# Optimization experiments

Hardware: AMD Instinct MI355X
Metric: run time of the kernel (lower is better)

## Reference

```python
import jax, jax.numpy as jnp
import numpy as np

B, S, E, H, FFN, NQ = 4, 2048, 1024, 16, 4096, 8
DK = E // H
EPS = 1e-5


def setup_inputs() -> dict:
    key = jax.random.key(0)
    ks = jax.random.split(key, 8)
    x = jax.random.normal(ks[0], (B, S, E), dtype=jnp.float32)
    theta = jax.random.normal(ks[1], (NQ,), dtype=jnp.float32)  # RY angles
    w1 = jax.random.normal(ks[2], (FFN, NQ), dtype=jnp.float32) / np.sqrt(NQ)
    b1 = jnp.zeros((FFN,), dtype=jnp.float32)
    w2 = jax.random.normal(ks[3], (E, FFN), dtype=jnp.float32) / np.sqrt(FFN)
    b2 = jnp.zeros((E,), dtype=jnp.float32)
    gamma1 = jnp.ones((E,), dtype=jnp.float32)
    beta1 = jnp.zeros((E,), dtype=jnp.float32)
    gamma2 = jnp.ones((E,), dtype=jnp.float32)
    beta2 = jnp.zeros((E,), dtype=jnp.float32)
    return {"x": x, "theta": theta, "w1": w1, "b1": b1, "w2": w2, "b2": b2,
            "gamma1": gamma1, "beta1": beta1, "gamma2": gamma2, "beta2": beta2}


def _layernorm(h, g, b):
    mu = jnp.mean(h, axis=-1, keepdims=True)
    var = jnp.mean(jnp.square(h - mu), axis=-1, keepdims=True)
    return (h - mu) * jax.lax.rsqrt(var + EPS) * g + b


def _attention(x):
    # q = k = v = separate_heads(x); no projection weights in the original.
    q = x.reshape(B, S, H, DK).transpose(0, 2, 1, 3)  # [B,H,S,DK]
    scores = jnp.einsum("bhqd,bhkd->bhqk", q, q) / np.sqrt(DK)
    probs = jax.nn.softmax(scores, axis=-1)
    out = jnp.einsum("bhqk,bhkd->bhqd", probs, q)
    return out.transpose(0, 2, 1, 3).reshape(B, S, E)


def _ffn_quantum(h, theta, w1, b1, w2, b2):
    # Per-token circuit: RX(x_i) then RY(theta_i) on independent qubits,
    # measure PauliZ -> <Z_i> = cos(x_i) * cos(theta_i). Batched over all tokens.
    qout = jnp.cos(h[..., :NQ]) * jnp.cos(theta)  # [B,S,NQ]
    hid = jax.nn.relu(jnp.einsum("bsq,fq->bsf", qout, w1) + b1)
    return jnp.einsum("bsf,ef->bse", hid, w2) + b2


def reference(x, theta, w1, b1, w2, b2, gamma1, beta1, gamma2, beta2):
    attn_out = _attention(x)
    h = _layernorm(x + attn_out, gamma1, beta1)
    ffn_out = _ffn_quantum(h, theta, w1, b1, w2, b2)
    return _layernorm(h + ffn_out, gamma2, beta2)
```

## Files before the change

kernel.cpp:

```cpp
#include <hip/hip_runtime.h>


#define Bq 4
#define Sq 2048
#define Eq 1024
#define Hq 16
#define DKq 64
#define FFNq 4096
#define NQq 8
#define LOG2E 1.44269504f

typedef unsigned int u32;
typedef unsigned short u16;
typedef _Float16 f16;
typedef f16 f16x8 __attribute__((ext_vector_type(8)));
typedef __fp16 fp16x2 __attribute__((ext_vector_type(2)));
typedef float f32x4 __attribute__((ext_vector_type(4)));

#if __has_builtin(__builtin_amdgcn_exp2f)
#define EXP2F __builtin_amdgcn_exp2f
#else
#define EXP2F exp2f
#endif

#define MFMA(a, b, c) __builtin_amdgcn_mfma_f32_16x16x32_f16((a), (b), (c), 0, 0, 0)

#define GLL(g, l)                                                          \
  __builtin_amdgcn_global_load_lds(                                        \
      (const __attribute__((address_space(1))) u32*)(g),                   \
      (__attribute__((address_space(3))) u32*)(l), 16, 0, 0)

__device__ __forceinline__ u16 f2h(float x) {
  f16 t = (f16)x;
  return __builtin_bit_cast(u16, t);
}
__device__ __forceinline__ float h2f(u16 w) {
  return (float)__builtin_bit_cast(f16, w);
}
#if __has_builtin(__builtin_amdgcn_cvt_pkrtz)
__device__ __forceinline__ u32 pkrtz(float a, float b) {
  fp16x2 r = __builtin_amdgcn_cvt_pkrtz(a, b);
  return __builtin_bit_cast(u32, r);
}
#else
__device__ __forceinline__ u32 pkrtz(float a, float b) {
  return (u32)f2h(a) | ((u32)f2h(b) << 16);
}
#endif

union F8 { f16x8 v; u32 w[4]; u16 h[8]; f16 e[8]; };

__global__ void k_cvt(const float* __restrict__ src, uint4* __restrict__ dst, int n8) {
  int i = blockIdx.x * 256 + threadIdx.x;
  if (i >= n8) return;
  const float4* s = (const float4*)src + 2 * (long)i;
  float4 a = s[0], b = s[1];
  uint4 r;
  r.x = pkrtz(a.x, a.y);
  r.y = pkrtz(a.z, a.w);
  r.z = pkrtz(b.x, b.y);
  r.w = pkrtz(b.z, b.w);
  dst[i] = r;
}

__global__ void k_prep(const float* __restrict__ x, u16* __restrict__ xh,
                       u16* __restrict__ xt) {
  __shared__ u16 tile[64 * 72];
  const int tid = threadIdx.x;
  const int bx = blockIdx.x;
  const int sb = bx & 31, bh = bx >> 5;
  const int b = bh >> 4, h = bh & 15;
  const int s0 = sb * 64;
  const int r = tid >> 2, cq = tid & 3;
  const float* xp = x + ((long)(b * Sq + s0 + r)) * Eq + h * 64 + cq * 16;
  float4 f0 = ((const float4*)xp)[0], f1 = ((const float4*)xp)[1];
  float4 f2 = ((const float4*)xp)[2], f3 = ((const float4*)xp)[3];
  u32 w[8];
  w[0] = pkrtz(f0.x, f0.y); w[1] = pkrtz(f0.z, f0.w);
  w[2] = pkrtz(f1.x, f1.y); w[3] = pkrtz(f1.z, f1.w);
  w[4] = pkrtz(f2.x, f2.y); w[5] = pkrtz(f2.z, f2.w);
  w[6] = pkrtz(f3.x, f3.y); w[7] = pkrtz(f3.z, f3.w);
  uint4* xo = (uint4*)(xh + ((long)(b * Sq + s0 + r)) * Eq + h * 64 + cq * 16);
  xo[0] = make_uint4(w[0], w[1], w[2], w[3]);
  xo[1] = make_uint4(w[4], w[5], w[6], w[7]);
  uint4* tp = (uint4*)(tile + r * 72 + cq * 16);
  tp[0] = make_uint4(w[0], w[1], w[2], w[3]);
  tp[1] = make_uint4(w[4], w[5], w[6], w[7]);
  __syncthreads();
  const int d = tid >> 2, rq = tid & 3;
  u32 o[8];
#pragma unroll
  for (int i = 0; i < 8; ++i) {
    u32 lo = tile[(rq * 16 + 2 * i) * 72 + d];
    u32 hi = tile[(rq * 16 + 2 * i + 1) * 72 + d];
    o[i] = lo | (hi << 16);
  }
  uint4* to = (uint4*)(xt + ((long)(bh * 64 + d)) * Sq + s0 + rq * 16);
  to[0] = make_uint4(o[0], o[1], o[2], o[3]);
  to[1] = make_uint4(o[4], o[5], o[6], o[7]);
}

__global__ __launch_bounds__(256, 2) void k_attn(const u16* __restrict__ xh,
                                                 const u16* __restrict__ xt,
                                                 u16* __restrict__ attn) {
  __shared__ __align__(16) u16 lds[32768];
  u16* Pl = lds + 16384;

  const int tid = threadIdx.x;
  const int wave = tid >> 6, lane = tid & 63;
  const int n = lane & 15, quad = lane >> 4;

  const int bx = blockIdx.x;
  const int qb = bx >> 6, bh = bx & 63;
  const int b = bh >> 4, h = bh & 15;

  const u16* xh_bh = xh + (long)b * Sq * Eq + h * 64;
  const u16* xt_bh = xt + (long)bh * 64 * Sq;

  const float SC = 0.125f * LOG2E;
  F8 qf[4][2];
  float shift[4], lrow[4] = {0.f, 0.f, 0.f, 0.f};
#pragma unroll
  for (int nt = 0; nt < 4; ++nt) {
    const int q = qb * 256 + wave * 64 + nt * 16 + n;
    const u16* qp = xh_bh + (long)q * Eq + quad * 8;
    F8 a, c;
    a.v = *(const f16x8*)qp;
    c.v = *(const f16x8*)(qp + 32);
    float s2 = 0.f;
#pragma unroll
    for (int i = 0; i < 8; ++i) {
      float va = (float)a.e[i], vc = (float)c.e[i];
      s2 += va * va + vc * vc;
      qf[nt][0].e[i] = a.e[i] * (f16)SC;
      qf[nt][1].e[i] = c.e[i] * (f16)SC;
    }
    s2 += __shfl_xor(s2, 16);
    s2 += __shfl_xor(s2, 32);
    shift[nt] = SC * s2;
  }

  const int r8 = lane >> 3;
  const int cl = (lane & 7) ^ r8;
  const u16* gK0 = xh_bh + (long)(wave * 16 + r8) * Eq + cl * 8;
  const u16* gK1 = gK0 + 8 * Eq;
  const u16* gV0 = xt_bh + (long)(wave * 16 + r8) * Sq + cl * 8;
  const u16* gV1 = gV0 + 8 * Sq;
  const int lK0 = wave * 1024, lK1 = lK0 + 512;
  const int lV0 = 4096 + wave * 1024, lV1 = lV0 + 512;

  u16* cur = lds;
  u16* nxt = lds + 8192;

  GLL(gK0, cur + lK0); GLL(gK1, cur + lK1);
  GLL(gV0, cur + lV0); GLL(gV1, cur + lV1);
  gK0 += 64 * Eq; gK1 += 64 * Eq; gV0 += 64; gV1 += 64;

  f32x4 O[4][4] = {};
  u16* Pw = Pl + wave * 4096;

  for (int kb = 0; kb < Sq / 64; ++kb) {
    __syncthreads();
    if (kb < Sq / 64 - 1) {
      GLL(gK0, nxt + lK0); GLL(gK1, nxt + lK1);
      GLL(gV0, nxt + lV0); GLL(gV1, nxt + lV1);
      gK0 += 64 * Eq; gK1 += 64 * Eq; gV0 += 64; gV1 += 64;
    }
    u16* Kl = cur;
    u16* Vt = cur + 4096;

    f32x4 ST[4][4];
#pragma unroll
    for (int nt = 0; nt < 4; ++nt) {
      const float ms = -shift[nt];
#pragma unroll
      for (int mt = 0; mt < 4; ++mt) {
        ST[nt][mt][0] = ms; ST[nt][mt][1] = ms;
        ST[nt][mt][2] = ms; ST[nt][mt][3] = ms;
      }
    }
#pragma unroll
    for (int mt = 0; mt < 4; ++mt) {
#pragma unroll
      for (int c = 0; c < 2; ++c) {
        f16x8 af = *(const f16x8*)(Kl + (mt * 16 + n) * 64 +
                                   (((c * 4 + quad) ^ (n & 7)) * 8));
#pragma unroll
        for (int nt = 0; nt < 4; ++nt)
          ST[nt][mt] = MFMA(af, qf[nt][c].v, ST[nt][mt]);
      }
    }

#pragma unroll
    for (int nt = 0; nt < 4; ++nt) {
      float ls = 0.f;
#pragma unroll
      for (int mt = 0; mt < 4; ++mt) {
        float p0 = EXP2F(ST[nt][mt][0]);
        float p1 = EXP2F(ST[nt][mt][1]);
        float p2 = EXP2F(ST[nt][mt][2]);
        float p3 = EXP2F(ST[nt][mt][3]);
        ls += (p0 + p1) + (p2 + p3);
        const int ch = 2 * mt + (quad >> 1);
        *(uint2*)(Pw + nt * 1024 + n * 64 + ((ch ^ (n & 7)) * 8) + (quad & 1) * 4) =
            make_uint2(pkrtz(p0, p1), pkrtz(p2, p3));
      }
      lrow[nt] += ls;
    }

#pragma unroll
    for (int c = 0; c < 2; ++c) {
      const int pc = ((c * 4 + quad) ^ (n & 7)) * 8;
      f16x8 pf[4];
#pragma unroll
      for (int nt = 0; nt < 4; ++nt)
        pf[nt] = *(const f16x8*)(Pw + nt * 1024 + n * 64 + pc);
#pragma unroll
      for (int dt = 0; dt < 4; ++dt) {
        f16x8 vf = *(const f16x8*)(Vt + (dt * 16 + n) * 64 + pc);
#pragma unroll
        for (int nt = 0; nt < 4; ++nt) O[nt][dt] = MFMA(vf, pf[nt], O[nt][dt]);
      }
    }
    u16* t = cur; cur = nxt; nxt = t;
  }

#pragma unroll
  for (int nt = 0; nt < 4; ++nt) {
    float l = lrow[nt];
    l += __shfl_xor(l, 16);
    l += __shfl_xor(l, 32);
    const float inv = 1.0f / l;
    const int q = qb * 256 + wave * 64 + nt * 16 + n;
    u16* op = attn + (long)b * Sq * Eq + (long)q * Eq + h * 64;
#pragma unroll
    for (int dt = 0; dt < 4; ++dt) {
      u32 w0 = pkrtz(O[nt][dt][0] * inv, O[nt][dt][1] * inv);
      u32 w1 = pkrtz(O[nt][dt][2] * inv, O[nt][dt][3] * inv);
      *(uint2*)(op + dt * 16 + quad * 4) = make_uint2(w0, w1);
    }
  }
}

__global__ void k_ln1(const u16* __restrict__ xh, const u16* __restrict__ attn,
                      const float* __restrict__ g, const float* __restrict__ be,
                      const float* __restrict__ theta, u16* __restrict__ hout,
                      u16* __restrict__ qout) {
  const long t = blockIdx.x;
  const int tid = threadIdx.x;
  uint2 xw = ((const uint2*)(xh + t * Eq))[tid];
  uint2 aw = ((const uint2*)(attn + t * Eq))[tid];
  float v0 = h2f(xw.x & 0xffff) + h2f(aw.x & 0xffff);
  float v1 = h2f(xw.x >> 16) + h2f(aw.x >> 16);
  float v2 = h2f(xw.y & 0xffff) + h2f(aw.y & 0xffff);
  float v3 = h2f(xw.y >> 16) + h2f(aw.y >> 16);
  float s = (v0 + v1) + (v2 + v3);
  float s2 = v0 * v0 + v1 * v1 + v2 * v2 + v3 * v3;
#pragma unroll
  for (int o = 1; o < 64; o <<= 1) {
    s += __shfl_xor(s, o);
    s2 += __shfl_xor(s2, o);
  }
  __shared__ float red[8];
  const int wv = tid >> 6, ln = tid & 63;
  if (ln == 0) { red[wv] = s; red[4 + wv] = s2; }
  __syncthreads();
  s = red[0] + red[1] + red[2] + red[3];
  s2 = red[4] + red[5] + red[6] + red[7];
  const float mu = s * (1.f / Eq);
  const float var = s2 * (1.f / Eq) - mu * mu;
  const float rstd = rsqrtf(var + 1e-5f);
  float4 gv = ((const float4*)g)[tid];
  float4 bv = ((const float4*)be)[tid];
  float o0 = (v0 - mu) * rstd * gv.x + bv.x;
  float o1 = (v1 - mu) * rstd * gv.y + bv.y;
  float o2 = (v2 - mu) * rstd * gv.z + bv.z;
  float o3 = (v3 - mu) * rstd * gv.w + bv.w;
  ((uint2*)(hout + t * Eq))[tid] = make_uint2(pkrtz(o0, o1), pkrtz(o2, o3));
  if (tid < 2) {
    float hv[4] = {o0, o1, o2, o3};
    float q[4];
#pragma unroll
    for (int i = 0; i < 4; ++i) q[i] = cosf(hv[i]) * cosf(theta[tid * 4 + i]);
    *(uint2*)(qout + t * NQq + tid * 4) = make_uint2(pkrtz(q[0], q[1]), pkrtz(q[2], q[3]));
  }
}

__global__ void k_hid(const u16* __restrict__ qout, const float* __restrict__ w1,
                      const float* __restrict__ b1, u16* __restrict__ hid) {
  __shared__ float qs[256][8];
  const int tid = threadIdx.x;
  const int fb = blockIdx.x & 63, tb = blockIdx.x >> 6;
  const int f0 = fb * 64, t0 = tb * 256;
  {
    uint4 qw = *(const uint4*)(qout + (long)(t0 + tid) * NQq);
    qs[tid][0] = h2f(qw.x & 0xffff); qs[tid][1] = h2f(qw.x >> 16);
    qs[tid][2] = h2f(qw.y & 0xffff); qs[tid][3] = h2f(qw.y >> 16);
    qs[tid][4] = h2f(qw.z & 0xffff); qs[tid][5] = h2f(qw.z >> 16);
    qs[tid][6] = h2f(qw.w & 0xffff); qs[tid][7] = h2f(qw.w >> 16);
  }
  __syncthreads();
  const int wave = tid >> 6, lane = tid & 63;
  const int f = f0 + lane;
  const float4* wp = (const float4*)(w1 + (long)f * NQq);
  float4 wa = wp[0], wb = wp[1];
  const float bb = b1[f];
  const int trow = wave * 64;
  u16* op = hid + (long)(t0 + trow) * FFNq + f;
#pragma unroll 4
  for (int i = 0; i < 64; ++i) {
    const float* q = qs[trow + i];
    float acc = bb + q[0] * wa.x + q[1] * wa.y + q[2] * wa.z + q[3] * wa.w +
                q[4] * wb.x + q[5] * wb.y + q[6] * wb.z + q[7] * wb.w;
    acc = fmaxf(acc, 0.f);
    op[(long)i * FFNq] = f2h(acc);
  }
}

__global__ __launch_bounds__(256, 2) void k_gemm(const u16* __restrict__ Ah,
                                                 const u16* __restrict__ Bh,
                                                 u16* __restrict__ C) {
  __shared__ __align__(16) u16 lds[32768];
  const int tid = threadIdx.x;
  const int wave = tid >> 6, lane = tid & 63;
  const int n = lane & 15, quad = lane >> 4;
  const int wm = wave >> 1, wn = wave & 1;
  const int m0 = (blockIdx.x >> 3) * 128;
  const int n0 = (blockIdx.x & 7) * 128;
  const int r8 = lane >> 3;
  const int cl = (lane & 7) ^ r8;

  const u16* gA[4];
  const u16* gB[4];
  int lA[4], lB[4];
#pragma unroll
  for (int j = 0; j < 4; ++j) {
    const int row = wave * 32 + j * 8;
    gA[j] = Ah + (long)(m0 + row + r8) * FFNq + cl * 8;
    gB[j] = Bh + (long)(n0 + row + r8) * FFNq + cl * 8;
    lA[j] = row * 64;
    lB[j] = 8192 + row * 64;
  }

  u16* cur = lds;
  u16* nxt = lds + 16384;

#pragma unroll
  for (int j = 0; j < 4; ++j) {
    GLL(gA[j], cur + lA[j]);
    GLL(gB[j], cur + lB[j]);
    gA[j] += 64;
    gB[j] += 64;
  }

  f32x4 acc[4][4] = {};
  for (int it = 0; it < FFNq / 64; ++it) {
    __syncthreads();
    if (it < FFNq / 64 - 1) {
#pragma unroll
      for (int j = 0; j < 4; ++j) {
        GLL(gA[j], nxt + lA[j]);
        GLL(gB[j], nxt + lB[j]);
        gA[j] += 64;
        gB[j] += 64;
      }
    }
    u16* La = cur;
    u16* Lb = cur + 8192;
#pragma unroll
    for (int c = 0; c < 2; ++c) {
      f16x8 af[4], bf[4];
#pragma unroll
      for (int i = 0; i < 4; ++i) {
        const int ra = wm * 64 + i * 16 + n;
        const int rb = wn * 64 + i * 16 + n;
        af[i] = *(const f16x8*)(La + ra * 64 + (((c * 4 + quad) ^ (n & 7)) * 8));
        bf[i] = *(const f16x8*)(Lb + rb * 64 + (((c * 4 + quad) ^ (n & 7)) * 8));
      }
#pragma unroll
      for (int i = 0; i < 4; ++i)
#pragma unroll
        for (int j = 0; j < 4; ++j) acc[i][j] = MFMA(af[i], bf[j], acc[i][j]);
    }
    u16* t = cur; cur = nxt; nxt = t;
  }
#pragma unroll
  for (int i = 0; i < 4; ++i) {
    const int row = m0 + wm * 64 + i * 16 + quad * 4;
#pragma unroll
    for (int j = 0; j < 4; ++j) {
      u16* cp = C + (long)row * Eq + n0 + wn * 64 + j * 16 + n;
      cp[0] = f2h(acc[i][j][0]);
      cp[Eq] = f2h(acc[i][j][1]);
      cp[2 * Eq] = f2h(acc[i][j][2]);
      cp[3 * Eq] = f2h(acc[i][j][3]);
    }
  }
}

__global__ void k_ln2(const u16* __restrict__ hin, const u16* __restrict__ ffn,
                      const float* __restrict__ b2, const float* __restrict__ g,
                      const float* __restrict__ be, float* __restrict__ out) {
  const long t = blockIdx.x;
  const int tid = threadIdx.x;
  uint2 hw = ((const uint2*)(hin + t * Eq))[tid];
  uint2 fw = ((const uint2*)(ffn + t * Eq))[tid];
  float4 b2v = ((const float4*)b2)[tid];
  float v0 = h2f(hw.x & 0xffff) + h2f(fw.x & 0xffff) + b2v.x;
  float v1 = h2f(hw.x >> 16) + h2f(fw.x >> 16) + b2v.y;
  float v2 = h2f(hw.y & 0xffff) + h2f(fw.y & 0xffff) + b2v.z;
  float v3 = h2f(hw.y >> 16) + h2f(fw.y >> 16) + b2v.w;
  float s = (v0 + v1) + (v2 + v3);
  float s2 = v0 * v0 + v1 * v1 + v2 * v2 + v3 * v3;
#pragma unroll
  for (int o = 1; o < 64; o <<= 1) {
    s += __shfl_xor(s, o);
    s2 += __shfl_xor(s2, o);
  }
  __shared__ float red[8];
  const int wv = tid >> 6, ln = tid & 63;
  if (ln == 0) { red[wv] = s; red[4 + wv] = s2; }
  __syncthreads();
  s = red[0] + red[1] + red[2] + red[3];
  s2 = red[4] + red[5] + red[6] + red[7];
  const float mu = s * (1.f / Eq);
  const float var = s2 * (1.f / Eq) - mu * mu;
  const float rstd = rsqrtf(var + 1e-5f);
  float4 gv = ((const float4*)g)[tid];
  float4 bv = ((const float4*)be)[tid];
  float4 o;
  o.x = (v0 - mu) * rstd * gv.x + bv.x;
  o.y = (v1 - mu) * rstd * gv.y + bv.y;
  o.z = (v2 - mu) * rstd * gv.z + bv.z;
  o.w = (v3 - mu) * rstd * gv.w + bv.w;
  ((float4*)(out + t * Eq))[tid] = o;
}

extern "C" void kernel_launch(void* const* d_in, const int* in_sizes, int n_in,
                              void* d_out, int out_size, void* d_ws, size_t ws_size,
                              hipStream_t stream) {
  const float* x = (const float*)d_in[0];
  const float* theta = (const float*)d_in[1];
  const float* w1 = (const float*)d_in[2];
  const float* b1 = (const float*)d_in[3];
  const float* w2 = (const float*)d_in[4];
  const float* b2 = (const float*)d_in[5];
  const float* g1 = (const float*)d_in[6];
  const float* be1 = (const float*)d_in[7];
  const float* g2 = (const float*)d_in[8];
  const float* be2 = (const float*)d_in[9];
  float* out = (float*)d_out;

  char* ws = (char*)d_ws;
  u16* attn = (u16*)(ws);
  u16* h = (u16*)(ws + 16777216);
  u16* xh = (u16*)(ws + 33554432);
  u16* xt = (u16*)(ws + 50331648);
  u16* ffn = (u16*)(ws + 67108864);
  u16* hid = (u16*)(ws + 83886080);
  u16* w2h = (u16*)(ws + 150994944);
  u16* qout = (u16*)(ws + 159383552);

  k_prep<<<Bq * Hq * (Sq / 64), 256, 0, stream>>>(x, xh, xt);
  k_cvt<<<2048, 256, 0, stream>>>(w2, (uint4*)w2h, (Eq * FFNq) / 8);
  k_attn<<<Bq * Hq * (Sq / 256), 256, 0, stream>>>(xh, xt, attn);
  k_ln1<<<Bq * Sq, 256, 0, stream>>>(xh, attn, g1, be1, theta, h, qout);
  k_hid<<<(Bq * Sq / 256) * (FFNq / 64), 256, 0, stream>>>(qout, w1, b1, hid);
  k_gemm<<<(Bq * Sq / 128) * (Eq / 128), 256, 0, stream>>>(hid, w2h, ffn);
  k_ln2<<<Bq * Sq, 256, 0, stream>>>(h, ffn, b2, g2, be2, out);
}
```

Measured before the change: 318.2 us.

## Split attention query tile across 8 waves and add MFMA priority hints

The attention kernel now launches 512 threads (8 waves) per block instead of 256, with each wave handling 32 query rows instead of 64. Per-wave registers for scores and outputs are halved, and each wave issues one K and one V global-to-LDS load per tile. s_setprio raises wave priority around the MFMA sections so matrix work interleaves with other waves' exp/softmax. The aim is more latency hiding and occupancy, at the cost of less K/V reuse per wave and more barrier participants.

```diff
diff --git a/kernel.cpp b/kernel.cpp
--- a/kernel.cpp
+++ b/kernel.cpp
@@ -100,7 +100,7 @@
   to[1] = make_uint4(o[4], o[5], o[6], o[7]);
 }
 
-__global__ __launch_bounds__(256, 2) void k_attn(const u16* __restrict__ xh,
+__global__ __launch_bounds__(512, 4) void k_attn(const u16* __restrict__ xh,
                                                  const u16* __restrict__ xt,
                                                  u16* __restrict__ attn) {
   __shared__ __align__(16) u16 lds[32768];
@@ -118,11 +118,11 @@
   const u16* xt_bh = xt + (long)bh * 64 * Sq;
 
   const float SC = 0.125f * LOG2E;
-  F8 qf[4][2];
-  float shift[4], lrow[4] = {0.f, 0.f, 0.f, 0.f};
-#pragma unroll
-  for (int nt = 0; nt < 4; ++nt) {
-    const int q = qb * 256 + wave * 64 + nt * 16 + n;
+  F8 qf[2][2];
+  float shift[2], lrow[2] = {0.f, 0.f};
+#pragma unroll
+  for (int nt = 0; nt < 2; ++nt) {
+    const int q = qb * 256 + wave * 32 + nt * 16 + n;
     const u16* qp = xh_bh + (long)q * Eq + quad * 8;
     F8 a, c;
     a.v = *(const f16x8*)qp;
@@ -142,36 +142,36 @@
 
   const int r8 = lane >> 3;
   const int cl = (lane & 7) ^ r8;
-  const u16* gK0 = xh_bh + (long)(wave * 16 + r8) * Eq + cl * 8;
-  const u16* gK1 = gK0 + 8 * Eq;
-  const u16* gV0 = xt_bh + (long)(wave * 16 + r8) * Sq + cl * 8;
-  const u16* gV1 = gV0 + 8 * Sq;
-  const int lK0 = wave * 1024, lK1 = lK0 + 512;
-  const int lV0 = 4096 + wave * 1024, lV1 = lV0 + 512;
+  const u16* gK = xh_bh + (long)(wave * 8 + r8) * Eq + cl * 8;
+  const u16* gV = xt_bh + (long)(wave * 8 + r8) * Sq + cl * 8;
+  const int lK = wave * 512;
+  const int lV = 4096 + wave * 512;
 
   u16* cur = lds;
   u16* nxt = lds + 8192;
 
-  GLL(gK0, cur + lK0); GLL(gK1, cur + lK1);
-  GLL(gV0, cur + lV0); GLL(gV1, cur + lV1);
-  gK0 += 64 * Eq; gK1 += 64 * Eq; gV0 += 64; gV1 += 64;
-
-  f32x4 O[4][4] = {};
-  u16* Pw = Pl + wave * 4096;
+  GLL(gK, cur + lK);
+  GLL(gV, cur + lV);
+  gK += 64 * Eq;
+  gV += 64;
+
+  f32x4 O[2][4] = {};
+  u16* Pw = Pl + wave * 2048;
 
   for (int kb = 0; kb < Sq / 64; ++kb) {
     __syncthreads();
     if (kb < Sq / 64 - 1) {
-      GLL(gK0, nxt + lK0); GLL(gK1, nxt + lK1);
-      GLL(gV0, nxt + lV0); GLL(gV1, nxt + lV1);
-      gK0 += 64 * Eq; gK1 += 64 * Eq; gV0 += 64; gV1 += 64;
+      GLL(gK, nxt + lK);
+      GLL(gV, nxt + lV);
+      gK += 64 * Eq;
+      gV += 64;
     }
     u16* Kl = cur;
     u16* Vt = cur + 4096;
 
-    f32x4 ST[4][4];
-#pragma unroll
-    for (int nt = 0; nt < 4; ++nt) {
+    f32x4 ST[2][4];
+#pragma unroll
+    for (int nt = 0; nt < 2; ++nt) {
       const float ms = -shift[nt];
 #pragma unroll
       for (int mt = 0; mt < 4; ++mt) {
@@ -179,6 +179,7 @@
         ST[nt][mt][2] = ms; ST[nt][mt][3] = ms;
       }
     }
+    __builtin_amdgcn_s_setprio(1);
 #pragma unroll
     for (int mt = 0; mt < 4; ++mt) {
 #pragma unroll
@@ -186,13 +187,14 @@
         f16x8 af = *(const f16x8*)(Kl + (mt * 16 + n) * 64 +
                                    (((c * 4 + quad) ^ (n & 7)) * 8));
 #pragma unroll
-        for (int nt = 0; nt < 4; ++nt)
+        for (int nt = 0; nt < 2; ++nt)
           ST[nt][mt] = MFMA(af, qf[nt][c].v, ST[nt][mt]);
       }
     }
-
-#pragma unroll
-    for (int nt = 0; nt < 4; ++nt) {
+    __builtin_amdgcn_s_setprio(0);
+
+#pragma unroll
+    for (int nt = 0; nt < 2; ++nt) {
       float ls = 0.f;
 #pragma unroll
       for (int mt = 0; mt < 4; ++mt) {
@@ -208,30 +210,32 @@
       lrow[nt] += ls;
     }
 
+    __builtin_amdgcn_s_setprio(1);
 #pragma unroll
     for (int c = 0; c < 2; ++c) {
       const int pc = ((c * 4 + quad) ^ (n & 7)) * 8;
-      f16x8 pf[4];
-#pragma unroll
-      for (int nt = 0; nt < 4; ++nt)
+      f16x8 pf[2];
+#pragma unroll
+      for (int nt = 0; nt < 2; ++nt)
         pf[nt] = *(const f16x8*)(Pw + nt * 1024 + n * 64 + pc);
 #pragma unroll
       for (int dt = 0; dt < 4; ++dt) {
         f16x8 vf = *(const f16x8*)(Vt + (dt * 16 + n) * 64 + pc);
 #pragma unroll
-        for (int nt = 0; nt < 4; ++nt) O[nt][dt] = MFMA(vf, pf[nt], O[nt][dt]);
-      }
-    }
+        for (int nt = 0; nt < 2; ++nt) O[nt][dt] = MFMA(vf, pf[nt], O[nt][dt]);
+      }
+    }
+    __builtin_amdgcn_s_setprio(0);
     u16* t = cur; cur = nxt; nxt = t;
   }
 
 #pragma unroll
-  for (int nt = 0; nt < 4; ++nt) {
+  for (int nt = 0; nt < 2; ++nt) {
     float l = lrow[nt];
     l += __shfl_xor(l, 16);
     l += __shfl_xor(l, 32);
     const float inv = 1.0f / l;
-    const int q = qb * 256 + wave * 64 + nt * 16 + n;
+    const int q = qb * 256 + wave * 32 + nt * 16 + n;
     u16* op = attn + (long)b * Sq * Eq + (long)q * Eq + h * 64;
 #pragma unroll
     for (int dt = 0; dt < 4; ++dt) {
@@ -463,7 +467,7 @@
 
   k_prep<<<Bq * Hq * (Sq / 64), 256, 0, stream>>>(x, xh, xt);
   k_cvt<<<2048, 256, 0, stream>>>(w2, (uint4*)w2h, (Eq * FFNq) / 8);
-  k_attn<<<Bq * Hq * (Sq / 256), 256, 0, stream>>>(xh, xt, attn);
+  k_attn<<<Bq * Hq * (Sq / 256), 512, 0, stream>>>(xh, xt, attn);
   k_ln1<<<Bq * Sq, 256, 0, stream>>>(xh, attn, g1, be1, theta, h, qout);
   k_hid<<<(Bq * Sq / 256) * (FFNq / 64), 256, 0, stream>>>(qout, w1, b1, hid);
   k_gemm<<<(Bq * Sq / 128) * (Eq / 128), 256, 0, stream>>>(hid, w2h, ffn);
```

Measured after the change: 311.1 us. 2.2% less time.
